# Kernel optimization log

Hardware: AMD Instinct MI355X
Metric: run time of the kernel (lower is better)

Reference implementation:

```python
import jax, jax.numpy as jnp
import numpy as np

B, S, E, H = 1, 4096, 768, 12
D = E // H  # head_dim = 64


def setup_inputs() -> dict:
    key = jax.random.key(0)
    ks = jax.random.split(key, 6)
    scale = 0.02
    x = jax.random.normal(ks[0], (B, S, E), dtype=jnp.float32)
    Wq = jax.random.normal(ks[1], (E, E), dtype=jnp.float32) * scale
    Wk = jax.random.normal(ks[2], (E, E), dtype=jnp.float32) * scale
    Wv = jax.random.normal(ks[3], (E, E), dtype=jnp.float32) * scale
    Wo = jax.random.normal(ks[4], (E, E), dtype=jnp.float32) * scale
    bo = jax.random.normal(ks[5], (E,), dtype=jnp.float32) * scale
    mask = jnp.tril(jnp.ones((S, S), dtype=bool))[None, None]  # [1,1,S,S] causal
    return {"x": x, "Wq": Wq, "Wk": Wk, "Wv": Wv, "Wo": Wo, "bo": bo, "mask": mask}


def reference(x, Wq, Wk, Wv, Wo, bo, mask):
    # projections (torch Linear: y = x @ W.T; here W stored as [E,E] applied as x@W)
    q = jnp.einsum('bse,ef->bsf', x, Wq).reshape(B, S, H, D).transpose(0, 2, 1, 3)
    k = jnp.einsum('bse,ef->bsf', x, Wk).reshape(B, S, H, D).transpose(0, 2, 1, 3)
    v = jnp.einsum('bse,ef->bsf', x, Wv).reshape(B, S, H, D).transpose(0, 2, 1, 3)
    scores = jnp.einsum('bhqd,bhkd->bhqk', q, k) / jnp.sqrt(jnp.float32(D))
    scores = jnp.where(mask, scores, -jnp.inf)
    attn = jax.nn.softmax(scores, axis=-1)  # dropout p=0 -> identity
    ctx = jnp.einsum('bhqk,bhkd->bhqd', attn, v)
    ctx = ctx.transpose(0, 2, 1, 3).reshape(B, S, E)
    return jnp.einsum('bse,ef->bsf', ctx, Wo) + bo
```

## Files before the change

### kernel.cpp

```cpp
#include <hip/hip_runtime.h>
#include <math.h>

#define S 4096
#define E 768
#define H 12
#define Dh 64
#define SCALE2 0.1803368801111204f

typedef short short8 __attribute__((ext_vector_type(8)));
typedef float floatx4 __attribute__((ext_vector_type(4)));

__device__ __forceinline__ unsigned short f2bf(float f) {
    union { float f; unsigned int i; } c; c.f = f;
    unsigned int i = c.i;
    return (unsigned short)((i + 0x7fffu + ((i >> 16) & 1u)) >> 16);
}

__device__ __forceinline__ unsigned int pk_bf16(float lo, float hi) {
#if __has_builtin(__builtin_amdgcn_cvt_pk_bf16_f32)
    typedef __bf16 bf16x2 __attribute__((ext_vector_type(2)));
    union { bf16x2 v; unsigned int u; } c;
    c.v = __builtin_amdgcn_cvt_pk_bf16_f32(lo, hi);
    return c.u;
#else
    union { float f; unsigned int i; } a, b; a.f = lo; b.f = hi;
    return ((a.i + 0x8000u) >> 16) | ((b.i + 0x8000u) & 0xFFFF0000u);
#endif
}

__device__ __forceinline__ void gload_lds16(const unsigned short* g, unsigned short* l) {
    __builtin_amdgcn_global_load_lds(
        (const __attribute__((address_space(1))) unsigned int*)g,
        (__attribute__((address_space(3))) unsigned int*)l, 16, 0, 0);
}

__global__ __launch_bounds__(256)
void convert_x(const float* __restrict__ src, unsigned short* __restrict__ dst) {
    int i = (blockIdx.x * 256 + threadIdx.x) * 8;
    float4 f0 = *reinterpret_cast<const float4*>(src + i);
    float4 f1 = *reinterpret_cast<const float4*>(src + i + 4);
    unsigned short u[8];
    u[0]=f2bf(f0.x); u[1]=f2bf(f0.y); u[2]=f2bf(f0.z); u[3]=f2bf(f0.w);
    u[4]=f2bf(f1.x); u[5]=f2bf(f1.y); u[6]=f2bf(f1.z); u[7]=f2bf(f1.w);
    *reinterpret_cast<uint4*>(dst + i) = *reinterpret_cast<uint4*>(u);
}

__global__ __launch_bounds__(256)
void transpose4(const float* __restrict__ s0, const float* __restrict__ s1,
                const float* __restrict__ s2, const float* __restrict__ s3,
                unsigned short* __restrict__ d0, unsigned short* __restrict__ d1,
                unsigned short* __restrict__ d2, unsigned short* __restrict__ d3) {
    __shared__ unsigned short tile[32][33];
    int z = blockIdx.z;
    const float* src = (z == 0) ? s0 : (z == 1) ? s1 : (z == 2) ? s2 : s3;
    unsigned short* dst = (z == 0) ? d0 : (z == 1) ? d1 : (z == 2) ? d2 : d3;
    int x = blockIdx.x * 32 + threadIdx.x;
    int y0 = blockIdx.y * 32;
    for (int j = threadIdx.y; j < 32; j += 8)
        tile[j][threadIdx.x] = f2bf(src[(size_t)(y0 + j) * E + x]);
    __syncthreads();
    int x2 = y0 + threadIdx.x;
    int y2 = blockIdx.x * 32;
    for (int j = threadIdx.y; j < 32; j += 8)
        dst[(size_t)(y2 + j) * E + x2] = tile[threadIdx.x][j];
}

__global__ __launch_bounds__(256)
void gemm_qkv(const unsigned short* __restrict__ A,
              const unsigned short* __restrict__ BT,
              unsigned short* __restrict__ Qb, unsigned short* __restrict__ Kb,
              unsigned short* __restrict__ VTb) {
    __shared__ unsigned short Asm[128 * 64];
    __shared__ unsigned short Bsm[64 * 64];
    const int tid  = threadIdx.x;
    const int wave = tid >> 6, lane = tid & 63;
    const int quad = lane >> 4, l16 = lane & 15;
    const int lrow = lane >> 3, lchunk = lane & 7;
    const int n0 = blockIdx.x * 64;
    const int m0 = blockIdx.y * 128;

    floatx4 acc[2][4];
    #pragma unroll
    for (int at = 0; at < 2; at++)
        #pragma unroll
        for (int ct = 0; ct < 4; ct++)
            #pragma unroll
            for (int r = 0; r < 4; r++) acc[at][ct][r] = 0.f;

    for (int k0 = 0; k0 < E; k0 += 64) {
        #pragma unroll
        for (int i = 0; i < 4; i++) {
            int rbase = wave * 32 + i * 8;
            int row   = rbase + lrow;
            int gc    = lchunk ^ (row & 7);
            gload_lds16(&A[(size_t)(m0 + row) * E + k0 + gc * 8], &Asm[rbase * 64]);
        }
        #pragma unroll
        for (int i = 0; i < 2; i++) {
            int rbase = wave * 16 + i * 8;
            int row   = rbase + lrow;
            int gc    = lchunk ^ (row & 7);
            gload_lds16(&BT[(size_t)(n0 + row) * E + k0 + gc * 8], &Bsm[rbase * 64]);
        }
        __syncthreads();
        #pragma unroll
        for (int kk = 0; kk < 2; kk++) {
            const int g = kk * 4 + quad;
            short8 af[2], bfr[4];
            #pragma unroll
            for (int t = 0; t < 2; t++) {
                int ar = wave * 32 + t * 16 + l16;
                af[t] = *reinterpret_cast<const short8*>(&Asm[ar * 64 + (g ^ (ar & 7)) * 8]);
            }
            #pragma unroll
            for (int ct = 0; ct < 4; ct++) {
                int br = ct * 16 + l16;
                bfr[ct] = *reinterpret_cast<const short8*>(&Bsm[br * 64 + (g ^ (br & 7)) * 8]);
            }
            #pragma unroll
            for (int at = 0; at < 2; at++)
                #pragma unroll
                for (int ct = 0; ct < 4; ct++)
                    acc[at][ct] = __builtin_amdgcn_mfma_f32_16x16x32_bf16(af[at], bfr[ct], acc[at][ct], 0, 0, 0);
        }
        __syncthreads();
    }

    const int sec  = n0 / 768;
    const int nb   = n0 - sec * 768;
    #pragma unroll
    for (int at = 0; at < 2; at++)
        #pragma unroll
        for (int ct = 0; ct < 4; ct++) {
            int nsec = nb + ct * 16 + l16, hh = nsec >> 6, d = nsec & 63;
            #pragma unroll
            for (int r = 0; r < 4; r++) {
                int s = m0 + wave * 32 + at * 16 + quad * 4 + r;
                float v = acc[at][ct][r];
                if (sec == 0)      Qb [(size_t)hh * S * Dh + (size_t)s * Dh + d] = f2bf(v * SCALE2);
                else if (sec == 1) Kb [(size_t)hh * S * Dh + (size_t)s * Dh + d] = f2bf(v);
                else               VTb[(size_t)hh * Dh * S + (size_t)d * S + s]  = f2bf(v);
            }
        }
}

__global__ __launch_bounds__(256)
void gemm_out(const float* __restrict__ ctxf,
              const unsigned short* __restrict__ BT,
              const float* __restrict__ lsumf,
              float* __restrict__ outp, const float* __restrict__ bias) {
    __shared__ unsigned short Asm[128 * 64];
    __shared__ unsigned short Bsm[64 * 64];
    const int tid  = threadIdx.x;
    const int wave = tid >> 6, lane = tid & 63;
    const int quad = lane >> 4, l16 = lane & 15;
    const int lrow = lane >> 3, lchunk = lane & 7;
    const int n0 = blockIdx.x * 64;
    const int m0 = blockIdx.y * 128;
    const int arow = tid >> 1, ahalf = tid & 1;

    floatx4 acc[2][4];
    #pragma unroll
    for (int at = 0; at < 2; at++)
        #pragma unroll
        for (int ct = 0; ct < 4; ct++)
            #pragma unroll
            for (int r = 0; r < 4; r++) acc[at][ct][r] = 0.f;

    for (int k0 = 0; k0 < E; k0 += 64) {
        {
            const float* asrc = ctxf + (size_t)(m0 + arow) * E + k0 + ahalf * 32;
            float linv = 1.0f / lsumf[(k0 >> 6) * S + m0 + arow];
            #pragma unroll
            for (int hf = 0; hf < 2; hf++) {
                float4 fa = *reinterpret_cast<const float4*>(asrc + hf * 16);
                float4 fb = *reinterpret_cast<const float4*>(asrc + hf * 16 + 4);
                float4 fc = *reinterpret_cast<const float4*>(asrc + hf * 16 + 8);
                float4 fd = *reinterpret_cast<const float4*>(asrc + hf * 16 + 12);
                uint4 w0, w1;
                w0.x = pk_bf16(fa.x * linv, fa.y * linv); w0.y = pk_bf16(fa.z * linv, fa.w * linv);
                w0.z = pk_bf16(fb.x * linv, fb.y * linv); w0.w = pk_bf16(fb.z * linv, fb.w * linv);
                w1.x = pk_bf16(fc.x * linv, fc.y * linv); w1.y = pk_bf16(fc.z * linv, fc.w * linv);
                w1.z = pk_bf16(fd.x * linv, fd.y * linv); w1.w = pk_bf16(fd.z * linv, fd.w * linv);
                int c0 = ahalf * 4 + hf * 2;
                *reinterpret_cast<uint4*>(&Asm[arow * 64 + ((c0    ) ^ (arow & 7)) * 8]) = w0;
                *reinterpret_cast<uint4*>(&Asm[arow * 64 + ((c0 + 1) ^ (arow & 7)) * 8]) = w1;
            }
        }
        #pragma unroll
        for (int i = 0; i < 2; i++) {
            int rbase = wave * 16 + i * 8;
            int row   = rbase + lrow;
            int gc    = lchunk ^ (row & 7);
            gload_lds16(&BT[(size_t)(n0 + row) * E + k0 + gc * 8], &Bsm[rbase * 64]);
        }
        __syncthreads();
        #pragma unroll
        for (int kk = 0; kk < 2; kk++) {
            const int g = kk * 4 + quad;
            short8 af[2], bfr[4];
            #pragma unroll
            for (int t = 0; t < 2; t++) {
                int ar = wave * 32 + t * 16 + l16;
                af[t] = *reinterpret_cast<const short8*>(&Asm[ar * 64 + (g ^ (ar & 7)) * 8]);
            }
            #pragma unroll
            for (int ct = 0; ct < 4; ct++) {
                int br = ct * 16 + l16;
                bfr[ct] = *reinterpret_cast<const short8*>(&Bsm[br * 64 + (g ^ (br & 7)) * 8]);
            }
            #pragma unroll
            for (int at = 0; at < 2; at++)
                #pragma unroll
                for (int ct = 0; ct < 4; ct++)
                    acc[at][ct] = __builtin_amdgcn_mfma_f32_16x16x32_bf16(af[at], bfr[ct], acc[at][ct], 0, 0, 0);
        }
        __syncthreads();
    }

    #pragma unroll
    for (int at = 0; at < 2; at++)
        #pragma unroll
        for (int ct = 0; ct < 4; ct++) {
            int n = n0 + ct * 16 + l16;
            float bn = bias[n];
            #pragma unroll
            for (int r = 0; r < 4; r++) {
                int s = m0 + wave * 32 + at * 16 + quad * 4 + r;
                outp[(size_t)s * E + n] = acc[at][ct][r] + bn;
            }
        }
}

__global__ __launch_bounds__(256)
void attn_kernel(const unsigned short* __restrict__ Q,
                 const unsigned short* __restrict__ K,
                 const unsigned short* __restrict__ VT,
                 float* __restrict__ ctxf,
                 float* __restrict__ lsumf) {
    __shared__ unsigned short Ksm[2][64 * 64];
    __shared__ unsigned short Vsm[2][64 * 64];
    __shared__ unsigned short P[4][2][16][72];
    const int tid  = threadIdx.x;
    const int wave = tid >> 6, lane = tid & 63;
    const int quad = lane >> 4, l16 = lane & 15;
    const int lrow = lane >> 3, lchunk = lane & 7;

    const int b = blockIdx.x;
    const int w = b / H;
    const int h = b - w * H;
    int Qb, ck, nck;
    if (w < 32)      { Qb = 31 - (w >> 2); ck = w & 3; nck = 4; }
    else if (w < 56) { int u = w - 32; int q = u / 3; Qb = 23 - q; ck = u - q * 3; nck = 3; }
    else if (w < 72) { int u = w - 56; Qb = 15 - (u >> 1); ck = u & 1; nck = 2; }
    else             { Qb = 7 - (w - 72); ck = 0; nck = 1; }
    const int ntiles = 2 * Qb + 2;
    const int kt0 = (ntiles * ck) / nck;
    const int kt1 = (ntiles * (ck + 1)) / nck;

    const int qs = Qb * 128 + wave * 32;

    const unsigned short* Qh = Q  + (size_t)h * S * Dh;
    const unsigned short* Kh = K  + (size_t)h * S * Dh;
    const unsigned short* Vh = VT + (size_t)h * Dh * S;

    short8 bq[2][2];
    #pragma unroll
    for (int st = 0; st < 2; st++)
        #pragma unroll
        for (int c = 0; c < 2; c++)
            bq[st][c] = *reinterpret_cast<const short8*>(
                &Qh[(size_t)(qs + st * 16 + l16) * Dh + c * 32 + quad * 8]);

    float lsum[2] = {0.f, 0.f};
    floatx4 o[2][4];
    #pragma unroll
    for (int st = 0; st < 2; st++)
        #pragma unroll
        for (int ct = 0; ct < 4; ct++)
            #pragma unroll
            for (int r = 0; r < 4; r++) o[st][ct][r] = 0.f;

    auto stage = [&](int kt, int buf) {
        #pragma unroll
        for (int i = 0; i < 2; i++) {
            int rbase = wave * 16 + i * 8;
            int row   = rbase + lrow;
            int gc    = lchunk ^ (row & 7);
            gload_lds16(&Kh[(size_t)(kt * 64 + row) * Dh + gc * 8], &Ksm[buf][rbase * 64]);
            gload_lds16(&Vh[(size_t)row * S + kt * 64 + gc * 8],    &Vsm[buf][rbase * 64]);
        }
    };

    stage(kt0, 0);
    __syncthreads();

    for (int kt = kt0; kt < kt1; kt++) {
        const int cur = (kt - kt0) & 1;
        if (kt + 1 < kt1) stage(kt + 1, cur ^ 1);

        floatx4 sc[2][4];
        #pragma unroll
        for (int st = 0; st < 2; st++)
            #pragma unroll
            for (int ct = 0; ct < 4; ct++)
                #pragma unroll
                for (int r = 0; r < 4; r++) sc[st][ct][r] = 0.f;
        #pragma unroll
        for (int c = 0; c < 2; c++)
            #pragma unroll
            for (int ct = 0; ct < 4; ct++) {
                int kr = ct * 16 + l16;
                short8 ak = *reinterpret_cast<const short8*>(
                    &Ksm[cur][kr * 64 + ((c * 4 + quad) ^ (kr & 7)) * 8]);
                sc[0][ct] = __builtin_amdgcn_mfma_f32_16x16x32_bf16(ak, bq[0][c], sc[0][ct], 0, 0, 0);
                sc[1][ct] = __builtin_amdgcn_mfma_f32_16x16x32_bf16(ak, bq[1][c], sc[1][ct], 0, 0, 0);
            }

        if (kt >= 2 * Qb) {
            #pragma unroll
            for (int st = 0; st < 2; st++) {
                int qrow = qs + st * 16 + l16;
                #pragma unroll
                for (int ct = 0; ct < 4; ct++)
                    #pragma unroll
                    for (int r = 0; r < 4; r++) {
                        int kcol = kt * 64 + ct * 16 + quad * 4 + r;
                        if (kcol > qrow) sc[st][ct][r] = -INFINITY;
                    }
            }
        }

        #pragma unroll
        for (int st = 0; st < 2; st++)
            #pragma unroll
            for (int ct = 0; ct < 4; ct++) {
                float pv[4];
                #pragma unroll
                for (int r = 0; r < 4; r++) {
                    float p = __builtin_amdgcn_exp2f(sc[st][ct][r]);
                    lsum[st] += p;
                    pv[r] = p;
                }
                uint2 w2;
                w2.x = pk_bf16(pv[0], pv[1]);
                w2.y = pk_bf16(pv[2], pv[3]);
                *reinterpret_cast<uint2*>(&P[wave][st][l16][ct * 16 + quad * 4]) = w2;
            }
        __asm__ volatile("s_waitcnt lgkmcnt(0)" ::: "memory");

        #pragma unroll
        for (int c = 0; c < 2; c++) {
            short8 ap0 = *reinterpret_cast<const short8*>(&P[wave][0][l16][c * 32 + quad * 8]);
            short8 ap1 = *reinterpret_cast<const short8*>(&P[wave][1][l16][c * 32 + quad * 8]);
            #pragma unroll
            for (int ct = 0; ct < 4; ct++) {
                int vr = ct * 16 + l16;
                short8 bv = *reinterpret_cast<const short8*>(
                    &Vsm[cur][vr * 64 + ((c * 4 + quad) ^ (vr & 7)) * 8]);
                o[0][ct] = __builtin_amdgcn_mfma_f32_16x16x32_bf16(ap0, bv, o[0][ct], 0, 0, 0);
                o[1][ct] = __builtin_amdgcn_mfma_f32_16x16x32_bf16(ap1, bv, o[1][ct], 0, 0, 0);
            }
        }
        __syncthreads();
    }

    #pragma unroll
    for (int st = 0; st < 2; st++) {
        lsum[st] += __shfl_xor(lsum[st], 16, 64);
        lsum[st] += __shfl_xor(lsum[st], 32, 64);
    }
    if (quad == 0) {
        #pragma unroll
        for (int st = 0; st < 2; st++)
            atomicAdd(&lsumf[h * S + qs + st * 16 + l16], lsum[st]);
    }
    #pragma unroll
    for (int st = 0; st < 2; st++)
        #pragma unroll
        for (int r = 0; r < 4; r++) {
            int s = qs + st * 16 + quad * 4 + r;
            #pragma unroll
            for (int ct = 0; ct < 4; ct++)
                atomicAdd(&ctxf[(size_t)s * E + h * Dh + ct * 16 + l16], o[st][ct][r]);
        }
}

extern "C" void kernel_launch(void* const* d_in, const int* in_sizes, int n_in,
                              void* d_out, int out_size, void* d_ws, size_t ws_size,
                              hipStream_t stream) {
    const float* x  = (const float*)d_in[0];
    const float* Wq = (const float*)d_in[1];
    const float* Wk = (const float*)d_in[2];
    const float* Wv = (const float*)d_in[3];
    const float* Wo = (const float*)d_in[4];
    const float* bo = (const float*)d_in[5];
    float* out = (float*)d_out;

    char* ws = (char*)d_ws;
    const size_t WT = (size_t)E * E * 2;
    const size_t QB = (size_t)S * E * 2;
    unsigned short* WqT = (unsigned short*)(ws + 0 * WT);
    unsigned short* WkT = (unsigned short*)(ws + 1 * WT);
    unsigned short* WvT = (unsigned short*)(ws + 2 * WT);
    unsigned short* WoT = (unsigned short*)(ws + 3 * WT);
    unsigned short* xb  = (unsigned short*)(ws + 4 * WT + 0 * QB);
    unsigned short* Qbf = (unsigned short*)(ws + 4 * WT + 1 * QB);
    unsigned short* Kbf = (unsigned short*)(ws + 4 * WT + 2 * QB);
    unsigned short* VTb = (unsigned short*)(ws + 4 * WT + 3 * QB);
    float*          ctxf  = (float*)(ws + 4 * WT + 4 * QB);
    float*          lsumf = (float*)(ws + 4 * WT + 4 * QB + (size_t)S * E * 4);

    hipMemsetAsync(ctxf,  0, (size_t)S * E * 4, stream);
    hipMemsetAsync(lsumf, 0, (size_t)H * S * 4, stream);

    convert_x<<<(S * E) / (256 * 8), 256, 0, stream>>>(x, xb);

    transpose4<<<dim3(24, 24, 4), dim3(32, 8), 0, stream>>>(Wq, Wk, Wv, Wo, WqT, WkT, WvT, WoT);

    gemm_qkv<<<dim3(36, 32), 256, 0, stream>>>(xb, WqT, Qbf, Kbf, VTb);

    attn_kernel<<<960, 256, 0, stream>>>(Qbf, Kbf, VTb, ctxf, lsumf);

    gemm_out<<<dim3(12, 32), 256, 0, stream>>>(ctxf, WoT, lsumf, out, bo);
}
```

Baseline: 246.8 us.

## Fuse prep kernels, XCD-aware GEMM tiling, finer attention split, drop double buffering

Merges the x conversion and weight transposes into one launch and combines the two memsets into one. Remaps the GEMM block indices so neighbouring tiles land on the same XCD, to improve L2 reuse. Splits the causal attention key range into up to 8 chunks per query block, giving 1728 blocks instead of 960, to balance load. Replaces the double-buffered K/V LDS staging with a single buffer, which lowers LDS use and may raise occupancy but gives up overlap of loads with compute. Finer splitting also adds more atomic accumulation traffic into ctx.

```diff
diff --git a/kernel.cpp b/kernel.cpp
--- a/kernel.cpp
+++ b/kernel.cpp
@@ -35,34 +35,38 @@
 }
 
 __global__ __launch_bounds__(256)
-void convert_x(const float* __restrict__ src, unsigned short* __restrict__ dst) {
-    int i = (blockIdx.x * 256 + threadIdx.x) * 8;
-    float4 f0 = *reinterpret_cast<const float4*>(src + i);
-    float4 f1 = *reinterpret_cast<const float4*>(src + i + 4);
-    unsigned short u[8];
-    u[0]=f2bf(f0.x); u[1]=f2bf(f0.y); u[2]=f2bf(f0.z); u[3]=f2bf(f0.w);
-    u[4]=f2bf(f1.x); u[5]=f2bf(f1.y); u[6]=f2bf(f1.z); u[7]=f2bf(f1.w);
-    *reinterpret_cast<uint4*>(dst + i) = *reinterpret_cast<uint4*>(u);
-}
-
-__global__ __launch_bounds__(256)
-void transpose4(const float* __restrict__ s0, const float* __restrict__ s1,
-                const float* __restrict__ s2, const float* __restrict__ s3,
-                unsigned short* __restrict__ d0, unsigned short* __restrict__ d1,
-                unsigned short* __restrict__ d2, unsigned short* __restrict__ d3) {
+void prep_kernel(const float* __restrict__ x, unsigned short* __restrict__ xb,
+                 const float* __restrict__ s0, const float* __restrict__ s1,
+                 const float* __restrict__ s2, const float* __restrict__ s3,
+                 unsigned short* __restrict__ d0, unsigned short* __restrict__ d1,
+                 unsigned short* __restrict__ d2, unsigned short* __restrict__ d3) {
     __shared__ unsigned short tile[32][33];
-    int z = blockIdx.z;
-    const float* src = (z == 0) ? s0 : (z == 1) ? s1 : (z == 2) ? s2 : s3;
-    unsigned short* dst = (z == 0) ? d0 : (z == 1) ? d1 : (z == 2) ? d2 : d3;
-    int x = blockIdx.x * 32 + threadIdx.x;
-    int y0 = blockIdx.y * 32;
-    for (int j = threadIdx.y; j < 32; j += 8)
-        tile[j][threadIdx.x] = f2bf(src[(size_t)(y0 + j) * E + x]);
-    __syncthreads();
-    int x2 = y0 + threadIdx.x;
-    int y2 = blockIdx.x * 32;
-    for (int j = threadIdx.y; j < 32; j += 8)
-        dst[(size_t)(y2 + j) * E + x2] = tile[threadIdx.x][j];
+    const int b = blockIdx.x;
+    const int tid = threadIdx.x;
+    if (b < 2304) {
+        int z = b / 576, rem = b - z * 576;
+        int bx = rem % 24, by = rem / 24;
+        const float* src = (z == 0) ? s0 : (z == 1) ? s1 : (z == 2) ? s2 : s3;
+        unsigned short* dst = (z == 0) ? d0 : (z == 1) ? d1 : (z == 2) ? d2 : d3;
+        int tx = tid & 31, ty = tid >> 5;
+        int xcol = bx * 32 + tx;
+        int y0 = by * 32;
+        for (int j = ty; j < 32; j += 8)
+            tile[j][tx] = f2bf(src[(size_t)(y0 + j) * E + xcol]);
+        __syncthreads();
+        int x2 = y0 + tx;
+        int y2 = bx * 32;
+        for (int j = ty; j < 32; j += 8)
+            dst[(size_t)(y2 + j) * E + x2] = tile[tx][j];
+    } else {
+        int i = ((b - 2304) * 256 + tid) * 8;
+        float4 f0 = *reinterpret_cast<const float4*>(x + i);
+        float4 f1 = *reinterpret_cast<const float4*>(x + i + 4);
+        unsigned short u[8];
+        u[0]=f2bf(f0.x); u[1]=f2bf(f0.y); u[2]=f2bf(f0.z); u[3]=f2bf(f0.w);
+        u[4]=f2bf(f1.x); u[5]=f2bf(f1.y); u[6]=f2bf(f1.z); u[7]=f2bf(f1.w);
+        *reinterpret_cast<uint4*>(xb + i) = *reinterpret_cast<uint4*>(u);
+    }
 }
 
 __global__ __launch_bounds__(256)
@@ -76,8 +80,12 @@
     const int wave = tid >> 6, lane = tid & 63;
     const int quad = lane >> 4, l16 = lane & 15;
     const int lrow = lane >> 3, lchunk = lane & 7;
-    const int n0 = blockIdx.x * 64;
-    const int m0 = blockIdx.y * 128;
+    const int bb = blockIdx.x;
+    const int xcd = bb & 7, j = bb >> 3;
+    const int mt = (xcd >> 1) * 8 + (j & 7);
+    const int nt = (xcd & 1) * 18 + (j >> 3);
+    const int n0 = nt * 64;
+    const int m0 = mt * 128;
 
     floatx4 acc[2][4];
     #pragma unroll
@@ -126,8 +134,8 @@
         __syncthreads();
     }
 
-    const int sec  = n0 / 768;
-    const int nb   = n0 - sec * 768;
+    const int sec = n0 / 768;
+    const int nb  = n0 - sec * 768;
     #pragma unroll
     for (int at = 0; at < 2; at++)
         #pragma unroll
@@ -155,8 +163,12 @@
     const int wave = tid >> 6, lane = tid & 63;
     const int quad = lane >> 4, l16 = lane & 15;
     const int lrow = lane >> 3, lchunk = lane & 7;
-    const int n0 = blockIdx.x * 64;
-    const int m0 = blockIdx.y * 128;
+    const int bb = blockIdx.x;
+    const int xcd = bb & 7, j = bb >> 3;
+    const int mt = (xcd >> 1) * 8 + (j & 7);
+    const int nt = (xcd & 1) * 6 + (j >> 3);
+    const int n0 = nt * 64;
+    const int m0 = mt * 128;
     const int arow = tid >> 1, ahalf = tid & 1;
 
     floatx4 acc[2][4];
@@ -238,8 +250,8 @@
                  const unsigned short* __restrict__ VT,
                  float* __restrict__ ctxf,
                  float* __restrict__ lsumf) {
-    __shared__ unsigned short Ksm[2][64 * 64];
-    __shared__ unsigned short Vsm[2][64 * 64];
+    __shared__ unsigned short Ksm[64 * 64];
+    __shared__ unsigned short Vsm[64 * 64];
     __shared__ unsigned short P[4][2][16][72];
     const int tid  = threadIdx.x;
     const int wave = tid >> 6, lane = tid & 63;
@@ -250,10 +262,14 @@
     const int w = b / H;
     const int h = b - w * H;
     int Qb, ck, nck;
-    if (w < 32)      { Qb = 31 - (w >> 2); ck = w & 3; nck = 4; }
-    else if (w < 56) { int u = w - 32; int q = u / 3; Qb = 23 - q; ck = u - q * 3; nck = 3; }
-    else if (w < 72) { int u = w - 56; Qb = 15 - (u >> 1); ck = u & 1; nck = 2; }
-    else             { Qb = 7 - (w - 72); ck = 0; nck = 1; }
+    if (w < 32)       { Qb = 31 - (w >> 3);       ck = w & 7;         nck = 8; }
+    else if (w < 60)  { int u = w - 32;  Qb = 27 - u / 7;  ck = u % 7; nck = 7; }
+    else if (w < 84)  { int u = w - 60;  Qb = 23 - u / 6;  ck = u % 6; nck = 6; }
+    else if (w < 104) { int u = w - 84;  Qb = 19 - u / 5;  ck = u % 5; nck = 5; }
+    else if (w < 120) { int u = w - 104; Qb = 15 - (u >> 2); ck = u & 3; nck = 4; }
+    else if (w < 132) { int u = w - 120; Qb = 11 - u / 3;  ck = u % 3; nck = 3; }
+    else if (w < 140) { int u = w - 132; Qb = 7 - (u >> 1); ck = u & 1; nck = 2; }
+    else              { Qb = 3 - (w - 140);       ck = 0;             nck = 1; }
     const int ntiles = 2 * Qb + 2;
     const int kt0 = (ntiles * ck) / nck;
     const int kt1 = (ntiles * (ck + 1)) / nck;
@@ -281,23 +297,16 @@
             #pragma unroll
             for (int r = 0; r < 4; r++) o[st][ct][r] = 0.f;
 
-    auto stage = [&](int kt, int buf) {
+    for (int kt = kt0; kt < kt1; kt++) {
         #pragma unroll
         for (int i = 0; i < 2; i++) {
             int rbase = wave * 16 + i * 8;
             int row   = rbase + lrow;
             int gc    = lchunk ^ (row & 7);
-            gload_lds16(&Kh[(size_t)(kt * 64 + row) * Dh + gc * 8], &Ksm[buf][rbase * 64]);
-            gload_lds16(&Vh[(size_t)row * S + kt * 64 + gc * 8],    &Vsm[buf][rbase * 64]);
-        }
-    };
-
-    stage(kt0, 0);
-    __syncthreads();
-
-    for (int kt = kt0; kt < kt1; kt++) {
-        const int cur = (kt - kt0) & 1;
-        if (kt + 1 < kt1) stage(kt + 1, cur ^ 1);
+            gload_lds16(&Kh[(size_t)(kt * 64 + row) * Dh + gc * 8], &Ksm[rbase * 64]);
+            gload_lds16(&Vh[(size_t)row * S + kt * 64 + gc * 8],    &Vsm[rbase * 64]);
+        }
+        __syncthreads();
 
         floatx4 sc[2][4];
         #pragma unroll
@@ -312,7 +321,7 @@
             for (int ct = 0; ct < 4; ct++) {
                 int kr = ct * 16 + l16;
                 short8 ak = *reinterpret_cast<const short8*>(
-                    &Ksm[cur][kr * 64 + ((c * 4 + quad) ^ (kr & 7)) * 8]);
+                    &Ksm[kr * 64 + ((c * 4 + quad) ^ (kr & 7)) * 8]);
                 sc[0][ct] = __builtin_amdgcn_mfma_f32_16x16x32_bf16(ak, bq[0][c], sc[0][ct], 0, 0, 0);
                 sc[1][ct] = __builtin_amdgcn_mfma_f32_16x16x32_bf16(ak, bq[1][c], sc[1][ct], 0, 0, 0);
             }
@@ -357,7 +366,7 @@
             for (int ct = 0; ct < 4; ct++) {
                 int vr = ct * 16 + l16;
                 short8 bv = *reinterpret_cast<const short8*>(
-                    &Vsm[cur][vr * 64 + ((c * 4 + quad) ^ (vr & 7)) * 8]);
+                    &Vsm[vr * 64 + ((c * 4 + quad) ^ (vr & 7)) * 8]);
                 o[0][ct] = __builtin_amdgcn_mfma_f32_16x16x32_bf16(ap0, bv, o[0][ct], 0, 0, 0);
                 o[1][ct] = __builtin_amdgcn_mfma_f32_16x16x32_bf16(ap1, bv, o[1][ct], 0, 0, 0);
             }
@@ -411,16 +420,14 @@
     float*          ctxf  = (float*)(ws + 4 * WT + 4 * QB);
     float*          lsumf = (float*)(ws + 4 * WT + 4 * QB + (size_t)S * E * 4);
 
-    hipMemsetAsync(ctxf,  0, (size_t)S * E * 4, stream);
-    hipMemsetAsync(lsumf, 0, (size_t)H * S * 4, stream);
-
-    convert_x<<<(S * E) / (256 * 8), 256, 0, stream>>>(x, xb);
-
-    transpose4<<<dim3(24, 24, 4), dim3(32, 8), 0, stream>>>(Wq, Wk, Wv, Wo, WqT, WkT, WvT, WoT);
-
-    gemm_qkv<<<dim3(36, 32), 256, 0, stream>>>(xb, WqT, Qbf, Kbf, VTb);
-
-    attn_kernel<<<960, 256, 0, stream>>>(Qbf, Kbf, VTb, ctxf, lsumf);
-
-    gemm_out<<<dim3(12, 32), 256, 0, stream>>>(ctxf, WoT, lsumf, out, bo);
-}
+    hipMemsetAsync(ctxf, 0, (size_t)S * E * 4 + (size_t)H * S * 4, stream);
+
+    prep_kernel<<<2304 + (S * E) / (256 * 8), 256, 0, stream>>>(
+        x, xb, Wq, Wk, Wv, Wo, WqT, WkT, WvT, WoT);
+
+    gemm_qkv<<<1152, 256, 0, stream>>>(xb, WqT, Qbf, Kbf, VTb);
+
+    attn_kernel<<<1728, 256, 0, stream>>>(Qbf, Kbf, VTb, ctxf, lsumf);
+
+    gemm_out<<<384, 256, 0, stream>>>(ctxf, WoT, lsumf, out, bo);
+}
```

Measured after the change: 252.3 us. 1.02x slower.
